# Kernel optimization log

Hardware: AMD Instinct MI355X
Metric: run time of the kernel (lower is better)

The kernel has to match this reference:

```python
import jax, jax.numpy as jnp
import numpy as np

TEMPERATURE = 10.0  # module init temperature (training mode)


def setup_inputs() -> dict:
    key = jax.random.key(0)
    kx, kg = jax.random.split(key)
    B, C, H, W = 64, 128, 64, 64
    n = C * H * W  # 524288
    x = jax.random.normal(kx, (B, C, H, W), dtype=jnp.float32)
    # Gumbel(0,1) noise for Gumbel-top-k sampling (== multinomial w/o replacement)
    u = jax.random.uniform(kg, (B, n), dtype=jnp.float32, minval=1e-20, maxval=1.0)
    gumbel = -jnp.log(-jnp.log(u))
    k = int(round(0.1 * n))  # percent_on * n = 52429
    return {"x": x, "gumbel": gumbel, "k": k}


def reference(x, gumbel, k):
    B = x.shape[0]
    n = x.shape[1] * x.shape[2] * x.shape[3]
    flat = x.reshape(B, n)                      # [B, n]
    logits = flat / TEMPERATURE
    # Categorical sampling of k winners without replacement == top-k of
    # gumbel-perturbed logits (equivalent to softmax(logits) + multinomial).
    _, idx = jax.lax.top_k(logits + gumbel, k)  # [B, k]
    mask = jnp.zeros((B, n), dtype=x.dtype).at[jnp.arange(B)[:, None], idx].set(1.0)
    out = (flat * mask).reshape(x.shape)
    return jnp.maximum(out, 0.0)  # relu=True
```

## Files before the change

kernel.cpp:

```cpp
#include <hip/hip_runtime.h>
#include <cstdint>

#define BROWS 64
#define NCOL  524288
#define CHUNKS 32
#define CHUNK  (NCOL / CHUNKS)
#define NV4    (CHUNK / 4)
#define LCAP   2048
#define ECAP   512
#define MAXCAP 24576
#define M_SAMP 32768
#define SEGS   128
#define SBLK   16
#define SLACK  5200
#define HB2    32768

typedef float nf4 __attribute__((ext_vector_type(4)));

#define ABV_OFF   0u
#define CCNT_OFF  256u
#define RINFO_OFF 512u
#define HIST_OFF  4096u
#define CAND_OFF  4096u
#define ZWORDS    (1024 + BROWS * HB2)

__device__ __forceinline__ uint32_t fkey(float s) {
  uint32_t b = __float_as_uint(s);
  return (b & 0x80000000u) ? ~b : (b | 0x80000000u);
}

__global__ __launch_bounds__(256) void k_zero(uint32_t* __restrict__ p, int n) {
  int i = blockIdx.x * 256 + threadIdx.x;
  if (i < n) p[i] = 0;
}

__global__ __launch_bounds__(256) void k_sampleA(const float* __restrict__ x,
                                                 const float* __restrict__ g,
                                                 uint32_t* __restrict__ hist) {
  int row = blockIdx.y;
  size_t rb = (size_t)row * NCOL;
  uint32_t* gh = hist + (size_t)row * HB2;
  int i0 = blockIdx.x * (M_SAMP / SBLK);
  for (int it = 0; it < (M_SAMP / SBLK) / 256; ++it) {
    int i = i0 + it * 256 + threadIdx.x;
    size_t off = rb + (size_t)(i >> 8) * (NCOL / SEGS) + (i & 255);
    uint32_t key = fkey(x[off] / 10.0f + g[off]);
    atomicAdd(&gh[key >> 17], 1u);
  }
}

__global__ __launch_bounds__(1024) void k_pick(const uint32_t* __restrict__ hist,
                                               const int* __restrict__ kptr,
                                               uint32_t* __restrict__ rinfo,
                                               uint32_t* __restrict__ abv,
                                               uint32_t* __restrict__ ccnt) {
  __shared__ uint32_t part[1024];
  __shared__ uint32_t segbuf[32];
  __shared__ uint32_t sel[4];
  int row = blockIdx.x;
  if (threadIdx.x == 0) { abv[row] = 0; ccnt[row] = 0; }
  const uint32_t* gh = hist + (size_t)row * HB2;
  const uint4* gh4 = (const uint4*)gh;
  uint32_t s = 0;
  #pragma unroll
  for (int j = 0; j < 8; ++j) {
    uint4 v = gh4[threadIdx.x * 8 + j];
    s += v.x + v.y + v.z + v.w;
  }
  part[threadIdx.x] = s;
  __syncthreads();
  if (threadIdx.x == 0) {
    uint32_t kk = (uint32_t)(*kptr);
    uint32_t rHi = ((kk > SLACK ? kk - SLACK : 0u) / 16u) + 1u;
    uint32_t rLo = ((kk + SLACK) / 16u) + 1u;
    if (rLo > M_SAMP) rLo = M_SAMP;
    uint32_t cum = 0, cumHi = 0, cumLo = 0;
    int segHi = -1, segLo = -1;
    for (int t = 1023; t >= 0; --t) {
      uint32_t c = part[t];
      if (segHi < 0 && cum + c >= rHi) { segHi = t; cumHi = cum; }
      if (segLo < 0 && cum + c >= rLo) { segLo = t; cumLo = cum; break; }
      cum += c;
    }
    if (segHi < 0) segHi = 0;
    if (segLo < 0) segLo = 0;
    sel[0] = (uint32_t)segHi; sel[1] = rHi - cumHi;
    sel[2] = (uint32_t)segLo; sel[3] = rLo - cumLo;
  }
  __syncthreads();
  int segHi = (int)sel[0], segLo = (int)sel[2];
  if (threadIdx.x < 32) segbuf[threadIdx.x] = gh[segHi * 32 + threadIdx.x];
  __syncthreads();
  if (threadIdx.x == 0) {
    uint32_t rem = sel[1], cum = 0;
    int bin = 0;
    for (int b = 31; b >= 0; --b) {
      uint32_t c = segbuf[b];
      if (cum + c >= rem) { bin = b; break; }
      cum += c;
    }
    uint32_t binHi = (uint32_t)(segHi * 32 + bin);
    rinfo[row * 4 + 0] = (binHi << 17) | 0x1FFFFu;
  }
  __syncthreads();
  if (threadIdx.x < 32) segbuf[threadIdx.x] = gh[segLo * 32 + threadIdx.x];
  __syncthreads();
  if (threadIdx.x == 0) {
    uint32_t rem = sel[3], cum = 0;
    int bin = 0;
    for (int b = 31; b >= 0; --b) {
      uint32_t c = segbuf[b];
      if (cum + c >= rem) { bin = b; break; }
      cum += c;
    }
    uint32_t binLo = (uint32_t)(segLo * 32 + bin);
    rinfo[row * 4 + 1] = binLo << 17;
  }
}

__global__ __launch_bounds__(256) void k_main(const float* __restrict__ x,
                                              const float* __restrict__ g,
                                              const uint32_t* __restrict__ rinfo,
                                              uint64_t* __restrict__ cand,
                                              uint32_t* __restrict__ ccnt,
                                              uint32_t* __restrict__ abv,
                                              float* __restrict__ out, int cap) {
  __shared__ uint64_t lbuf[LCAP];
  __shared__ uint32_t lcnt, lbase;
  __shared__ uint32_t wsum[4];
  int row = blockIdx.y, chunk = blockIdx.x;
  uint32_t keyHi = rinfo[row * 4 + 0];
  uint32_t keyLo = rinfo[row * 4 + 1];
  if (threadIdx.x == 0) lcnt = 0;
  __syncthreads();
  size_t base = (size_t)row * NCOL + (size_t)chunk * CHUNK;
  const float4* x4 = (const float4*)(x + base);
  const float4* g4 = (const float4*)(g + base);
  nf4* o4 = (nf4*)(out + base);
  uint32_t mycnt = 0;

#define PROC(a, b, i)                                                          \
  {                                                                            \
    uint32_t f0 = fkey(a.x / 10.0f + b.x);                                     \
    uint32_t f1 = fkey(a.y / 10.0f + b.y);                                     \
    uint32_t f2 = fkey(a.z / 10.0f + b.z);                                     \
    uint32_t f3 = fkey(a.w / 10.0f + b.w);                                     \
    nf4 o;                                                                     \
    o.x = (f0 > keyHi) ? fmaxf(a.x, 0.0f) : 0.0f;                              \
    o.y = (f1 > keyHi) ? fmaxf(a.y, 0.0f) : 0.0f;                              \
    o.z = (f2 > keyHi) ? fmaxf(a.z, 0.0f) : 0.0f;                              \
    o.w = (f3 > keyHi) ? fmaxf(a.w, 0.0f) : 0.0f;                              \
    __builtin_nontemporal_store(o, &o4[i]);                                    \
    mycnt += (f0 > keyHi) + (f1 > keyHi) + (f2 > keyHi) + (f3 > keyHi);        \
    uint32_t li = (uint32_t)(chunk * CHUNK + (i) * 4);                         \
    if (f0 >= keyLo && f0 <= keyHi) { uint32_t p = atomicAdd(&lcnt, 1u); if (p < LCAP) lbuf[p] = ((uint64_t)f0 << 32) | li; }        \
    if (f1 >= keyLo && f1 <= keyHi) { uint32_t p = atomicAdd(&lcnt, 1u); if (p < LCAP) lbuf[p] = ((uint64_t)f1 << 32) | (li + 1u); } \
    if (f2 >= keyLo && f2 <= keyHi) { uint32_t p = atomicAdd(&lcnt, 1u); if (p < LCAP) lbuf[p] = ((uint64_t)f2 << 32) | (li + 2u); } \
    if (f3 >= keyLo && f3 <= keyHi) { uint32_t p = atomicAdd(&lcnt, 1u); if (p < LCAP) lbuf[p] = ((uint64_t)f3 << 32) | (li + 3u); } \
  }

  for (int ii = 0; ii < NV4 / 1024; ++ii) {
    int i0 = ii * 1024 + threadIdx.x;
    float4 a0 = x4[i0];
    float4 a1 = x4[i0 + 256];
    float4 a2 = x4[i0 + 512];
    float4 a3 = x4[i0 + 768];
    float4 b0 = g4[i0];
    float4 b1 = g4[i0 + 256];
    float4 b2 = g4[i0 + 512];
    float4 b3 = g4[i0 + 768];
    PROC(a0, b0, i0)
    PROC(a1, b1, i0 + 256)
    PROC(a2, b2, i0 + 512)
    PROC(a3, b3, i0 + 768)
  }
#undef PROC

  for (int off = 32; off > 0; off >>= 1) mycnt += __shfl_down(mycnt, off);
  int lane = threadIdx.x & 63, wid = threadIdx.x >> 6;
  if (lane == 0) wsum[wid] = mycnt;
  __syncthreads();
  if (threadIdx.x == 0) {
    atomicAdd(&abv[row], wsum[0] + wsum[1] + wsum[2] + wsum[3]);
    lbase = atomicAdd(&ccnt[row], lcnt < LCAP ? lcnt : (uint32_t)LCAP);
  }
  __syncthreads();
  uint32_t cnt = lcnt < LCAP ? lcnt : (uint32_t)LCAP;
  uint64_t* dst = cand + (size_t)row * (size_t)cap;
  for (uint32_t i = threadIdx.x; i < cnt; i += 256) {
    uint32_t p = lbase + i;
    if (p < (uint32_t)cap) dst[p] = lbuf[i];
  }
}

__global__ __launch_bounds__(256) void k_finalize(const float* __restrict__ x,
                                                  const uint64_t* __restrict__ cand,
                                                  const uint32_t* __restrict__ ccnt,
                                                  const uint32_t* __restrict__ abv,
                                                  const uint32_t* __restrict__ rinfo,
                                                  const int* __restrict__ kptr,
                                                  float* __restrict__ out, int cap) {
  __shared__ uint32_t h[4096];
  __shared__ uint32_t part[256];
  __shared__ uint64_t elist[ECAP];
  __shared__ uint32_t ecnt;
  __shared__ int s_cut, s_need2;
  int row = blockIdx.x;
  uint32_t m = ccnt[row];
  if (m > (uint32_t)cap) m = (uint32_t)cap;
  int need = (int)((uint32_t)(*kptr)) - (int)abv[row];
  if (need <= 0) return;
  size_t rb = (size_t)row * NCOL;
  const uint64_t* c = cand + (size_t)row * (size_t)cap;
  if ((uint32_t)need >= m) {
    for (uint32_t i = threadIdx.x; i < m; i += 256) {
      uint32_t idx = (uint32_t)c[i];
      out[rb + idx] = fmaxf(x[rb + idx], 0.0f);
    }
    return;
  }
  uint32_t keyLo = rinfo[row * 4 + 1];
  uint32_t range = rinfo[row * 4 + 0] - keyLo;
  int bits = 32 - __clz((int)(range | 1u));
  int shift = bits > 12 ? bits - 12 : 0;
  for (int i = threadIdx.x; i < 4096; i += 256) h[i] = 0;
  if (threadIdx.x == 0) ecnt = 0;
  __syncthreads();
  for (uint32_t i = threadIdx.x; i < m; i += 256) {
    uint32_t key = (uint32_t)(c[i] >> 32);
    atomicAdd(&h[(key - keyLo) >> shift], 1u);
  }
  __syncthreads();
  uint32_t s = 0;
  for (int j = 0; j < 16; ++j) s += h[threadIdx.x * 16 + j];
  part[threadIdx.x] = s;
  __syncthreads();
  if (threadIdx.x == 0) {
    uint32_t cum = 0;
    int seg = 255;
    for (; seg > 0; --seg) {
      if (cum + part[seg] >= (uint32_t)need) break;
      cum += part[seg];
    }
    int bin = seg * 16 + 15;
    for (; bin > seg * 16; --bin) {
      if (cum + h[bin] >= (uint32_t)need) break;
      cum += h[bin];
    }
    s_cut = bin;
    s_need2 = need - (int)cum;
  }
  __syncthreads();
  int cut = s_cut, need2 = s_need2;
  for (uint32_t i = threadIdx.x; i < m; i += 256) {
    uint64_t e = c[i];
    int bin = (int)(((uint32_t)(e >> 32) - keyLo) >> shift);
    if (bin > cut) {
      uint32_t idx = (uint32_t)e;
      out[rb + idx] = fmaxf(x[rb + idx], 0.0f);
    } else if (bin == cut) {
      uint32_t p = atomicAdd(&ecnt, 1u);
      if (p < ECAP) elist[p] = e ^ 0xFFFFFFFFull;
    }
  }
  __syncthreads();
  int mm = (int)(ecnt < (uint32_t)ECAP ? ecnt : (uint32_t)ECAP);
  for (int pass = 0; pass < mm; ++pass) {
    for (int i = threadIdx.x; 2 * i + (pass & 1) + 1 < mm; i += 256) {
      int a2 = 2 * i + (pass & 1);
      uint64_t va = elist[a2], vb = elist[a2 + 1];
      if (vb > va) { elist[a2] = vb; elist[a2 + 1] = va; }
    }
    __syncthreads();
  }
  int w = need2 < mm ? need2 : mm;
  for (int i = threadIdx.x; i < w; i += 256) {
    uint32_t idx = ~(uint32_t)elist[i];
    out[rb + idx] = fmaxf(x[rb + idx], 0.0f);
  }
}

extern "C" void kernel_launch(void* const* d_in, const int* in_sizes, int n_in,
                              void* d_out, int out_size, void* d_ws, size_t ws_size,
                              hipStream_t stream) {
  const float* x = (const float*)d_in[0];
  const float* g = (const float*)d_in[1];
  const int* kptr = (const int*)d_in[2];
  float* out = (float*)d_out;
  char* ws = (char*)d_ws;

  uint32_t* abv = (uint32_t*)(ws + ABV_OFF);
  uint32_t* ccnt = (uint32_t*)(ws + CCNT_OFF);
  uint32_t* rinfo = (uint32_t*)(ws + RINFO_OFF);
  uint32_t* hist = (uint32_t*)(ws + HIST_OFF);
  uint64_t* cand = (uint64_t*)(ws + CAND_OFF);

  long cap_avail = ((long)ws_size - (long)CAND_OFF) / (8 * BROWS);
  int cap = cap_avail < MAXCAP ? (int)cap_avail : MAXCAP;
  if (cap < 1) cap = 1;

  k_zero<<<(ZWORDS + 255) / 256, 256, 0, stream>>>((uint32_t*)ws, ZWORDS);
  dim3 sgrid(SBLK, BROWS);
  k_sampleA<<<sgrid, 256, 0, stream>>>(x, g, hist);
  k_pick<<<BROWS, 1024, 0, stream>>>(hist, kptr, rinfo, abv, ccnt);
  dim3 grid(CHUNKS, BROWS);
  k_main<<<grid, 256, 0, stream>>>(x, g, rinfo, cand, ccnt, abv, out, cap);
  k_finalize<<<BROWS, 256, 0, stream>>>(x, cand, ccnt, abv, rinfo, kptr, out, cap);
}
```

Measured before the change: 210.6 us.

## Aggregate candidate pushes per wavefront, store candidate values, double chunk count

Replaces the per-element shared-memory atomic used to append boundary candidates with a wavefront ballot, so one leader lane reserves space for all of its wave's candidates. Each candidate's relu'd value is now stored next to it in workspace, so finalize no longer does a random gather from x. The grid is split into twice as many chunks per row and the local candidate buffer is halved. The changes trade extra workspace traffic and a smaller per-block candidate capacity for less atomic contention and more parallelism.

```diff
diff --git a/kernel.cpp b/kernel.cpp
--- a/kernel.cpp
+++ b/kernel.cpp
@@ -3,10 +3,10 @@
 
 #define BROWS 64
 #define NCOL  524288
-#define CHUNKS 32
+#define CHUNKS 64
 #define CHUNK  (NCOL / CHUNKS)
 #define NV4    (CHUNK / 4)
-#define LCAP   2048
+#define LCAP   1024
 #define ECAP   512
 #define MAXCAP 24576
 #define M_SAMP 32768
@@ -122,10 +122,12 @@
                                               const float* __restrict__ g,
                                               const uint32_t* __restrict__ rinfo,
                                               uint64_t* __restrict__ cand,
+                                              float* __restrict__ cval,
                                               uint32_t* __restrict__ ccnt,
                                               uint32_t* __restrict__ abv,
                                               float* __restrict__ out, int cap) {
   __shared__ uint64_t lbuf[LCAP];
+  __shared__ float lval[LCAP];
   __shared__ uint32_t lcnt, lbase;
   __shared__ uint32_t wsum[4];
   int row = blockIdx.y, chunk = blockIdx.x;
@@ -133,11 +135,27 @@
   uint32_t keyLo = rinfo[row * 4 + 1];
   if (threadIdx.x == 0) lcnt = 0;
   __syncthreads();
+  int lane = threadIdx.x & 63;
   size_t base = (size_t)row * NCOL + (size_t)chunk * CHUNK;
   const float4* x4 = (const float4*)(x + base);
   const float4* g4 = (const float4*)(g + base);
   nf4* o4 = (nf4*)(out + base);
   uint32_t mycnt = 0;
+
+#define PUSH(cond, key, idx, val)                                              \
+  {                                                                            \
+    uint64_t mset = __ballot(cond);                                            \
+    if (mset) {                                                                \
+      int leader = (int)__ffsll((long long)mset) - 1;                          \
+      uint32_t bse = 0;                                                        \
+      if (lane == leader) bse = atomicAdd(&lcnt, (uint32_t)__popcll(mset));    \
+      bse = __shfl(bse, leader);                                               \
+      if (cond) {                                                              \
+        uint32_t p = bse + (uint32_t)__popcll(mset & ((1ull << lane) - 1ull)); \
+        if (p < LCAP) { lbuf[p] = ((uint64_t)(key) << 32) | (idx); lval[p] = (val); } \
+      }                                                                        \
+    }                                                                          \
+  }
 
 #define PROC(a, b, i)                                                          \
   {                                                                            \
@@ -153,10 +171,14 @@
     __builtin_nontemporal_store(o, &o4[i]);                                    \
     mycnt += (f0 > keyHi) + (f1 > keyHi) + (f2 > keyHi) + (f3 > keyHi);        \
     uint32_t li = (uint32_t)(chunk * CHUNK + (i) * 4);                         \
-    if (f0 >= keyLo && f0 <= keyHi) { uint32_t p = atomicAdd(&lcnt, 1u); if (p < LCAP) lbuf[p] = ((uint64_t)f0 << 32) | li; }        \
-    if (f1 >= keyLo && f1 <= keyHi) { uint32_t p = atomicAdd(&lcnt, 1u); if (p < LCAP) lbuf[p] = ((uint64_t)f1 << 32) | (li + 1u); } \
-    if (f2 >= keyLo && f2 <= keyHi) { uint32_t p = atomicAdd(&lcnt, 1u); if (p < LCAP) lbuf[p] = ((uint64_t)f2 << 32) | (li + 2u); } \
-    if (f3 >= keyLo && f3 <= keyHi) { uint32_t p = atomicAdd(&lcnt, 1u); if (p < LCAP) lbuf[p] = ((uint64_t)f3 << 32) | (li + 3u); } \
+    bool c0 = (f0 >= keyLo) && (f0 <= keyHi);                                  \
+    bool c1 = (f1 >= keyLo) && (f1 <= keyHi);                                  \
+    bool c2 = (f2 >= keyLo) && (f2 <= keyHi);                                  \
+    bool c3 = (f3 >= keyLo) && (f3 <= keyHi);                                  \
+    PUSH(c0, f0, li, fmaxf(a.x, 0.0f))                                         \
+    PUSH(c1, f1, li + 1u, fmaxf(a.y, 0.0f))                                    \
+    PUSH(c2, f2, li + 2u, fmaxf(a.z, 0.0f))                                    \
+    PUSH(c3, f3, li + 3u, fmaxf(a.w, 0.0f))                                    \
   }
 
   for (int ii = 0; ii < NV4 / 1024; ++ii) {
@@ -175,9 +197,10 @@
     PROC(a3, b3, i0 + 768)
   }
 #undef PROC
+#undef PUSH
 
   for (int off = 32; off > 0; off >>= 1) mycnt += __shfl_down(mycnt, off);
-  int lane = threadIdx.x & 63, wid = threadIdx.x >> 6;
+  int wid = threadIdx.x >> 6;
   if (lane == 0) wsum[wid] = mycnt;
   __syncthreads();
   if (threadIdx.x == 0) {
@@ -187,14 +210,16 @@
   __syncthreads();
   uint32_t cnt = lcnt < LCAP ? lcnt : (uint32_t)LCAP;
   uint64_t* dst = cand + (size_t)row * (size_t)cap;
+  float* dv = cval + (size_t)row * (size_t)cap;
   for (uint32_t i = threadIdx.x; i < cnt; i += 256) {
     uint32_t p = lbase + i;
-    if (p < (uint32_t)cap) dst[p] = lbuf[i];
+    if (p < (uint32_t)cap) { dst[p] = lbuf[i]; dv[p] = lval[i]; }
   }
 }
 
 __global__ __launch_bounds__(256) void k_finalize(const float* __restrict__ x,
                                                   const uint64_t* __restrict__ cand,
+                                                  const float* __restrict__ cval,
                                                   const uint32_t* __restrict__ ccnt,
                                                   const uint32_t* __restrict__ abv,
                                                   const uint32_t* __restrict__ rinfo,
@@ -212,10 +237,11 @@
   if (need <= 0) return;
   size_t rb = (size_t)row * NCOL;
   const uint64_t* c = cand + (size_t)row * (size_t)cap;
+  const float* cv = cval + (size_t)row * (size_t)cap;
   if ((uint32_t)need >= m) {
     for (uint32_t i = threadIdx.x; i < m; i += 256) {
       uint32_t idx = (uint32_t)c[i];
-      out[rb + idx] = fmaxf(x[rb + idx], 0.0f);
+      out[rb + idx] = cv[i];
     }
     return;
   }
@@ -256,8 +282,7 @@
     uint64_t e = c[i];
     int bin = (int)(((uint32_t)(e >> 32) - keyLo) >> shift);
     if (bin > cut) {
-      uint32_t idx = (uint32_t)e;
-      out[rb + idx] = fmaxf(x[rb + idx], 0.0f);
+      out[rb + (uint32_t)e] = cv[i];
     } else if (bin == cut) {
       uint32_t p = atomicAdd(&ecnt, 1u);
       if (p < ECAP) elist[p] = e ^ 0xFFFFFFFFull;
@@ -295,15 +320,16 @@
   uint32_t* hist = (uint32_t*)(ws + HIST_OFF);
   uint64_t* cand = (uint64_t*)(ws + CAND_OFF);
 
-  long cap_avail = ((long)ws_size - (long)CAND_OFF) / (8 * BROWS);
+  long cap_avail = ((long)ws_size - (long)CAND_OFF) / (12 * BROWS);
   int cap = cap_avail < MAXCAP ? (int)cap_avail : MAXCAP;
   if (cap < 1) cap = 1;
+  float* cval = (float*)(ws + CAND_OFF + (size_t)BROWS * (size_t)cap * 8u);
 
   k_zero<<<(ZWORDS + 255) / 256, 256, 0, stream>>>((uint32_t*)ws, ZWORDS);
   dim3 sgrid(SBLK, BROWS);
   k_sampleA<<<sgrid, 256, 0, stream>>>(x, g, hist);
   k_pick<<<BROWS, 1024, 0, stream>>>(hist, kptr, rinfo, abv, ccnt);
   dim3 grid(CHUNKS, BROWS);
-  k_main<<<grid, 256, 0, stream>>>(x, g, rinfo, cand, ccnt, abv, out, cap);
-  k_finalize<<<BROWS, 256, 0, stream>>>(x, cand, ccnt, abv, rinfo, kptr, out, cap);
-}
+  k_main<<<grid, 256, 0, stream>>>(x, g, rinfo, cand, cval, ccnt, abv, out, cap);
+  k_finalize<<<BROWS, 256, 0, stream>>>(x, cand, cval, ccnt, abv, rinfo, kptr, out, cap);
+}
```

New measurement: 209.5 us. About the same (-0.5%).
